# Optimization experiments

Hardware: AMD Instinct MI355X
Metric: run time of the kernel (lower is better)

## Reference

```python
import jax, jax.numpy as jnp
import numpy as np

N_CLASSES = 3  # hardcoded in the original module (labels == 0/1/2)
EPS = 1e-12    # F.normalize default eps


def setup_inputs() -> dict:
    key = jax.random.key(0)
    k1, k2, k3 = jax.random.split(key, 3)
    query = jax.random.normal(k1, (32768, 256), dtype=jnp.float32)
    memory = jax.random.normal(k2, (3, 512, 256), dtype=jnp.float32)
    labels = jax.random.randint(k3, (32768,), 0, 3, dtype=jnp.int64)
    return {"query": query, "labels": labels, "memory": memory}


def reference(query, labels, memory):
    C, n_cells, d = memory.shape  # (3, 512, 256)
    # ---- read: cross-attention over all C*n_cells memory slots ----
    mem_flat = memory.reshape(C * n_cells, d)
    scores = jax.nn.softmax(query @ mem_flat.T, axis=1)  # (N, C*n_cells)
    q_read = scores @ mem_flat                           # (N, d) == the per-row loop, batched

    # ---- update (training path): masked softmax over queries per class ----
    def upd(c):
        mask = labels == c                               # (N,)
        logits = query @ memory[c].T                     # (N, n_cells)
        logits = jnp.where(mask[:, None], logits, -jnp.inf)
        sq = jax.nn.softmax(logits, axis=0)              # softmax over (masked) queries
        delta = sq.T @ query                             # (n_cells, d); zero rows contribute 0
        new = memory[c] + delta
        norm = jnp.maximum(jnp.linalg.norm(new, axis=1, keepdims=True), EPS)
        return new / norm                                # F.normalize over dim=1

    new_mem = jnp.stack([upd(c) for c in range(C)])      # C is a small fixed constant (3)
    return q_read, jax.lax.stop_gradient(new_mem)        # original detaches updated memory
```

## Files before the change

kernel.cpp:

```cpp
#include <hip/hip_runtime.h>
#include <math.h>

#define NQ    32768
#define DDIM  256
#define NCLS  3
#define CELLS 512
#define STOT  1536
#define BK    32

typedef __attribute__((ext_vector_type(8)))  short bf16x8;
typedef __attribute__((ext_vector_type(16))) float f32x16;

#define ROWF(r) (((r) & 3) + 8 * ((r) >> 2) + 4 * lh)

#define PIPE_WAIT_BAR(N) asm volatile("s_waitcnt vmcnt(" #N ")\n\ts_barrier" ::: "memory")
#define PIPE_BAR()       asm volatile("s_barrier" ::: "memory")

__device__ __forceinline__ f32x16 mfma16(bf16x8 a, bf16x8 b, f32x16 c) {
    return __builtin_amdgcn_mfma_f32_32x32x16_bf16(a, b, c, 0, 0, 0);
}
__device__ __forceinline__ unsigned short f2bf(float f) {
    const unsigned u = __float_as_uint(f);
    return (unsigned short)((u + 0x7FFFu + ((u >> 16) & 1u)) >> 16);
}
__device__ __forceinline__ float bf2f(unsigned short b) {
    return __uint_as_float(((unsigned)b) << 16);
}
__device__ __forceinline__ void gl16(const unsigned short* g, unsigned short* l) {
    __builtin_amdgcn_global_load_lds(
        (const __attribute__((address_space(1))) unsigned int*)g,
        (__attribute__((address_space(3))) unsigned int*)l, 16, 0, 0);
}

__global__ __launch_bounds__(256) void k_convert(const float* __restrict__ src,
        unsigned short* __restrict__ hi, unsigned short* __restrict__ lo,
        unsigned short* __restrict__ hiT, float* __restrict__ sq, int R) {
    __shared__ unsigned short lh_s[64][65];
    const int r0 = blockIdx.x * 64, k0 = blockIdx.y * 64, t = threadIdx.x;
#pragma unroll
    for (int it = 0; it < 4; ++it) {
        const int idx = t + 256 * it;
        const int rl = idx >> 4, kq = idx & 15;
        const float4 v = *(const float4*)(src + (size_t)(r0 + rl) * DDIM + k0 + kq * 4);
        const unsigned short h0 = f2bf(v.x), h1 = f2bf(v.y), h2 = f2bf(v.z), h3 = f2bf(v.w);
        const unsigned short l0 = f2bf(v.x - bf2f(h0)), l1 = f2bf(v.y - bf2f(h1));
        const unsigned short l2 = f2bf(v.z - bf2f(h2)), l3 = f2bf(v.w - bf2f(h3));
        ushort4 hv; hv.x = h0; hv.y = h1; hv.z = h2; hv.w = h3;
        ushort4 lv; lv.x = l0; lv.y = l1; lv.z = l2; lv.w = l3;
        *(ushort4*)(hi + (size_t)(r0 + rl) * DDIM + k0 + kq * 4) = hv;
        *(ushort4*)(lo + (size_t)(r0 + rl) * DDIM + k0 + kq * 4) = lv;
        lh_s[rl][kq * 4 + 0] = h0; lh_s[rl][kq * 4 + 1] = h1;
        lh_s[rl][kq * 4 + 2] = h2; lh_s[rl][kq * 4 + 3] = h3;
        float ssq = v.x * v.x + v.y * v.y + v.z * v.z + v.w * v.w;
        ssq += __shfl_xor(ssq, 1, 64);
        ssq += __shfl_xor(ssq, 2, 64);
        ssq += __shfl_xor(ssq, 4, 64);
        ssq += __shfl_xor(ssq, 8, 64);
        if (kq == 0) atomicAdd(&sq[r0 + rl], ssq);
    }
    __syncthreads();
#pragma unroll
    for (int it = 0; it < 16; ++it) {
        const int idx = t + 256 * it;
        const int kl = idx >> 6, rl = idx & 63;
        hiT[(size_t)(k0 + kl) * R + r0 + rl] = lh_s[rl][kl];
    }
}

__global__ __launch_bounds__(256) void k_pe(
        const unsigned short* __restrict__ Qhi, const unsigned short* __restrict__ Qlo,
        const unsigned short* __restrict__ Mhi, const unsigned short* __restrict__ Mlo,
        const int* __restrict__ labels, const float* __restrict__ qn2,
        const float* __restrict__ mn2,
        unsigned short* __restrict__ P, unsigned short* __restrict__ ET,
        int ibase, int ch, int ipg) {
    __shared__ unsigned short smem[2][2][2][128][BK];
    typedef unsigned short trt[32][40];
    trt* trP = (trt*)&smem[0][0][0][0][0];
    trt* trE = trP + 4;

    const int t = threadIdx.x, lane = t & 63, wid = t >> 6;
    const int l31 = lane & 31, lh = lane >> 5;
    const int wi = wid >> 1, wj = wid & 1;
    int ib, jb;
    if (ipg > 0) {
        const int xcd = blockIdx.x & 7, s = blockIdx.x >> 3;
        jb = s % 12; ib = xcd * ipg + s / 12;
    } else { jb = blockIdx.x % 12; ib = blockIdx.x / 12; }
    const int iblk = ib * 128, jblk = jb * 128;
    const int iloc0 = iblk + wi * 64;
    const int j0    = jblk + wj * 64;
    const int cblk  = jb >> 2;

    const int c0 = wid * 128 + lane, c1 = c0 + 64;
    const int r0 = c0 >> 2, o0 = ((c0 ^ (c0 >> 3)) & 3) * 8;
    const int r1 = c1 >> 2, o1 = ((c1 ^ (c1 >> 3)) & 3) * 8;
    const unsigned short* gA[2] = { Qhi + (size_t)(ibase + iblk) * DDIM,
                                    Qlo + (size_t)(ibase + iblk) * DDIM };
    const unsigned short* gB[2] = { Mhi + (size_t)jblk * DDIM,
                                    Mlo + (size_t)jblk * DDIM };
    auto STAGE = [&](int b, int k0) {
#pragma unroll
        for (int h = 0; h < 2; ++h) {
            gl16(gA[h] + (size_t)r0 * DDIM + k0 + o0, &smem[b][0][h][0][0] + c0 * 8);
            gl16(gA[h] + (size_t)r1 * DDIM + k0 + o1, &smem[b][0][h][0][0] + c1 * 8);
            gl16(gB[h] + (size_t)r0 * DDIM + k0 + o0, &smem[b][1][h][0][0] + c0 * 8);
            gl16(gB[h] + (size_t)r1 * DDIM + k0 + o1, &smem[b][1][h][0][0] + c1 * 8);
        }
    };

    f32x16 acc[2][2] = {};
    const int ra0 = wi * 64 + l31, ra1 = ra0 + 32;
    const int rb0 = wj * 64 + l31, rb1 = rb0 + 32;
    const int swa = (ra0 >> 1) & 3;
    const int swb = (rb0 >> 1) & 3;
    auto COMPUTE = [&](int b) {
#pragma unroll
        for (int t16 = 0; t16 < 2; ++t16) {
            const int oc = t16 * 2 + lh;
            const int ka = (oc ^ swa) * 8, kb = (oc ^ swb) * 8;
            const bf16x8 a0h = *(const bf16x8*)&smem[b][0][0][ra0][ka];
            const bf16x8 a1h = *(const bf16x8*)&smem[b][0][0][ra1][ka];
            const bf16x8 a0l = *(const bf16x8*)&smem[b][0][1][ra0][ka];
            const bf16x8 a1l = *(const bf16x8*)&smem[b][0][1][ra1][ka];
            const bf16x8 b0h = *(const bf16x8*)&smem[b][1][0][rb0][kb];
            const bf16x8 b1h = *(const bf16x8*)&smem[b][1][0][rb1][kb];
            const bf16x8 b0l = *(const bf16x8*)&smem[b][1][1][rb0][kb];
            const bf16x8 b1l = *(const bf16x8*)&smem[b][1][1][rb1][kb];
            acc[0][0] = mfma16(a0h, b0h, acc[0][0]);
            acc[0][0] = mfma16(a0h, b0l, acc[0][0]);
            acc[0][0] = mfma16(a0l, b0h, acc[0][0]);
            acc[0][1] = mfma16(a0h, b1h, acc[0][1]);
            acc[0][1] = mfma16(a0h, b1l, acc[0][1]);
            acc[0][1] = mfma16(a0l, b1h, acc[0][1]);
            acc[1][0] = mfma16(a1h, b0h, acc[1][0]);
            acc[1][0] = mfma16(a1h, b0l, acc[1][0]);
            acc[1][0] = mfma16(a1l, b0h, acc[1][0]);
            acc[1][1] = mfma16(a1h, b1h, acc[1][1]);
            acc[1][1] = mfma16(a1h, b1l, acc[1][1]);
            acc[1][1] = mfma16(a1l, b1h, acc[1][1]);
        }
    };

    STAGE(0, 0);
    STAGE(1, BK);
    for (int s = 0; s < DDIM / BK - 1; ++s) {
        PIPE_WAIT_BAR(8);
        COMPUTE(s & 1);
        PIPE_BAR();
        if (s + 2 < DDIM / BK) STAGE(s & 1, (s + 2) * BK);
    }
    PIPE_WAIT_BAR(0);
    COMPUTE(1);
    __syncthreads();

#pragma unroll
    for (int ti = 0; ti < 2; ++ti) {
        float qn[16]; unsigned lm = 0;
        const int ig0 = ibase + iloc0 + ti * 32;
#pragma unroll
        for (int r = 0; r < 16; ++r) {
            const int ir = ig0 + ROWF(r);
            qn[r] = 6.0f * sqrtf(qn2[ir]);
            lm |= (unsigned)(labels[ir] == cblk) << r;
        }
#pragma unroll
        for (int tj = 0; tj < 2; ++tj) {
            const int jg = j0 + tj * 32 + l31;
            const float mn = 6.0f * sqrtf(mn2[jg]);
#pragma unroll
            for (int r = 0; r < 16; ++r) {
                const float lg = acc[ti][tj][r];
                trP[wid][ROWF(r)][l31] = f2bf(__expf(lg - qn[r]));
                const float e = ((lm >> r) & 1u) ? __expf(lg - mn) : 0.0f;
                trE[wid][l31][ROWF(r)] = f2bf(e);
            }
            const int rr = lane >> 1, off = (lane & 1) * 16;
            {
                const unsigned short* lp = &trP[wid][rr][off];
                const bf16x8 w0 = *(const bf16x8*)(lp);
                const bf16x8 w1 = *(const bf16x8*)(lp + 8);
                unsigned short* prow = P + (size_t)(iloc0 + ti * 32 + rr) * STOT
                                         + j0 + tj * 32 + off;
                *(bf16x8*)(prow)     = w0;
                *(bf16x8*)(prow + 8) = w1;
            }
            {
                const unsigned short* lp = &trE[wid][rr][off];
                const bf16x8 w0 = *(const bf16x8*)(lp);
                const bf16x8 w1 = *(const bf16x8*)(lp + 8);
                unsigned short* erow = ET + (size_t)(j0 + tj * 32 + rr) * ch
                                          + iloc0 + ti * 32 + off;
                *(bf16x8*)(erow)     = w0;
                *(bf16x8*)(erow + 8) = w1;
            }
        }
    }
}

__global__ __launch_bounds__(256) void k_pv(const unsigned short* __restrict__ P,
        const unsigned short* __restrict__ MhiT,
        float* __restrict__ out, int ibase) {
    __shared__ unsigned short sP[2][64][64];
    __shared__ unsigned short sV[2][128][64];
    const int t = threadIdx.x, lane = t & 63, wid = t >> 6;
    const int l31 = lane & 31, lh = lane >> 5;
    const int wq = wid >> 1, wd = wid & 1;
    const int qblk = blockIdx.x * 64, dblk = blockIdx.y * 128;
    const int d0 = dblk + wd * 64;
    const unsigned short* gP = P + (size_t)qblk * STOT;
    const unsigned short* gV = MhiT + (size_t)dblk * STOT;

    auto STAGE = [&](int b, int k0) {
#pragma unroll
        for (int it = 0; it < 2; ++it) {
            const int c = wid * 128 + it * 64 + lane;
            const int r = c >> 3, o = ((c & 7) ^ (r & 7)) * 8;
            gl16(gP + (size_t)r * STOT + k0 + o, &sP[b][0][0] + c * 8);
        }
#pragma unroll
        for (int it = 0; it < 4; ++it) {
            const int c = wid * 256 + it * 64 + lane;
            const int r = c >> 3, o = ((c & 7) ^ (r & 7)) * 8;
            gl16(gV + (size_t)r * STOT + k0 + o, &sV[b][0][0] + c * 8);
        }
    };

    bf16x8 bones;
    const short ob = (l31 == 0) ? (short)0x3F80 : (short)0;
#pragma unroll
    for (int e = 0; e < 8; ++e) bones[e] = ob;

    f32x16 acc[2] = {};
    f32x16 accS = {};
    const int rp = wq * 32 + l31, rv0 = wd * 64 + l31, rv1 = rv0 + 32;
    auto COMPUTE = [&](int b) {
#pragma unroll
        for (int t16 = 0; t16 < 4; ++t16) {
            const int oc = t16 * 2 + lh;
            const bf16x8 a0 = *(const bf16x8*)&sP[b][rp][(oc ^ (rp & 7)) * 8];
            const bf16x8 b0 = *(const bf16x8*)&sV[b][rv0][(oc ^ (rv0 & 7)) * 8];
            const bf16x8 b1 = *(const bf16x8*)&sV[b][rv1][(oc ^ (rv1 & 7)) * 8];
            acc[0] = mfma16(a0, b0, acc[0]);
            acc[1] = mfma16(a0, b1, acc[1]);
            accS   = mfma16(a0, bones, accS);
        }
    };

    STAGE(0, 0);
    STAGE(1, 64);
    for (int s = 0; s < STOT / 64 - 1; ++s) {
        PIPE_WAIT_BAR(6);
        COMPUTE(s & 1);
        PIPE_BAR();
        if (s + 2 < STOT / 64) STAGE(s & 1, (s + 2) * 64);
    }
    PIPE_WAIT_BAR(0);
    COMPUTE(1);

    float rinv[16];
#pragma unroll
    for (int r = 0; r < 16; ++r) rinv[r] = 1.f / __shfl(accS[r], lh << 5, 64);
#pragma unroll
    for (int td = 0; td < 2; ++td) {
#pragma unroll
        for (int r = 0; r < 16; ++r) {
            const int ig = ibase + qblk + wq * 32 + ROWF(r);
            out[(size_t)ig * DDIM + d0 + td * 32 + l31] = acc[td][r] * rinv[r];
        }
    }
}

__global__ __launch_bounds__(256) void k_delta4(const unsigned short* __restrict__ ET,
        const unsigned short* __restrict__ QhiT,
        float* __restrict__ delta, float* __restrict__ colsum,
        int ibase, int ch, int ppx) {
    __shared__ unsigned short sE[2][128][64];
    __shared__ unsigned short sQ[2][128][64];
    const int t = threadIdx.x, lane = t & 63, wid = t >> 6;
    const int l31 = lane & 31, lh = lane >> 5;
    const int wj = wid >> 1, wd = wid & 1;
    int jb, db, kb;
    if (ppx > 0) {
        const int xcd = blockIdx.x & 7, s = blockIdx.x >> 3;
        jb = s % 12;
        const int pidx = xcd * ppx + s / 12;
        kb = pidx >> 1; db = pidx & 1;
    } else {
        jb = blockIdx.x % 12; db = (blockIdx.x / 12) & 1; kb = blockIdx.x / 24;
    }
    const int jblk = jb * 128, dblk = db * 128, i0 = kb * 1024;
    const int j0 = jblk + wj * 64, d0 = dblk + wd * 64;
    const unsigned short* gE = ET + (size_t)jblk * ch + i0;
    const unsigned short* gQ = QhiT + (size_t)dblk * NQ + ibase + i0;

    auto STAGE = [&](int b, int k0) {
#pragma unroll
        for (int it = 0; it < 4; ++it) {
            const int c = wid * 256 + it * 64 + lane;
            const int r = c >> 3, o = ((c & 7) ^ (r & 7)) * 8;
            gl16(gE + (size_t)r * ch + k0 + o, &sE[b][0][0] + c * 8);
            gl16(gQ + (size_t)r * NQ + k0 + o, &sQ[b][0][0] + c * 8);
        }
    };

    bf16x8 bones;
    const short ob = (l31 == 0) ? (short)0x3F80 : (short)0;
#pragma unroll
    for (int e = 0; e < 8; ++e) bones[e] = ob;

    f32x16 acc[2][2] = {};
    f32x16 accS0 = {}, accS1 = {};
    const int re0 = wj * 64 + l31, re1 = re0 + 32;
    const int rq0 = wd * 64 + l31, rq1 = rq0 + 32;
    auto COMPUTE = [&](int b) {
#pragma unroll
        for (int t16 = 0; t16 < 4; ++t16) {
            const int oc = t16 * 2 + lh;
            const bf16x8 a0 = *(const bf16x8*)&sE[b][re0][(oc ^ (re0 & 7)) * 8];
            const bf16x8 a1 = *(const bf16x8*)&sE[b][re1][(oc ^ (re1 & 7)) * 8];
            const bf16x8 b0 = *(const bf16x8*)&sQ[b][rq0][(oc ^ (rq0 & 7)) * 8];
            const bf16x8 b1 = *(const bf16x8*)&sQ[b][rq1][(oc ^ (rq1 & 7)) * 8];
            acc[0][0] = mfma16(a0, b0, acc[0][0]);
            acc[0][1] = mfma16(a0, b1, acc[0][1]);
            acc[1][0] = mfma16(a1, b0, acc[1][0]);
            acc[1][1] = mfma16(a1, b1, acc[1][1]);
            if (wd == 0) {
                accS0 = mfma16(a0, bones, accS0);
                accS1 = mfma16(a1, bones, accS1);
            }
        }
    };

    STAGE(0, 0);
    STAGE(1, 64);
    for (int s = 0; s < 15; ++s) {
        PIPE_WAIT_BAR(8);
        COMPUTE(s & 1);
        PIPE_BAR();
        if (s + 2 < 16) STAGE(s & 1, (s + 2) * 64);
    }
    PIPE_WAIT_BAR(0);
    COMPUTE(1);

#pragma unroll
    for (int tj = 0; tj < 2; ++tj) {
#pragma unroll
        for (int td = 0; td < 2; ++td) {
#pragma unroll
            for (int r = 0; r < 16; ++r) {
                const int jr = j0 + tj * 32 + ROWF(r);
                atomicAdd(&delta[(size_t)jr * DDIM + d0 + td * 32 + l31], acc[tj][td][r]);
            }
        }
    }
    if (wd == 0 && l31 == 0) {
#pragma unroll
        for (int r = 0; r < 16; ++r) {
            atomicAdd(&colsum[j0 + ROWF(r)], accS0[r]);
            atomicAdd(&colsum[j0 + 32 + ROWF(r)], accS1[r]);
        }
    }
}

__global__ void k_final(const float* __restrict__ M,
                        const float* __restrict__ delta,
                        const float* __restrict__ colsum,
                        float* __restrict__ out) {
    const int row  = blockIdx.x * 4 + (threadIdx.x >> 6);
    const int lane = threadIdx.x & 63;
    const float inv = 1.f / colsum[row];
    const float4 mv = *(const float4*)(M + (size_t)row * DDIM + lane * 4);
    const float4 dv = *(const float4*)(delta + (size_t)row * DDIM + lane * 4);
    float4 nv;
    nv.x = fmaf(dv.x, inv, mv.x);
    nv.y = fmaf(dv.y, inv, mv.y);
    nv.z = fmaf(dv.z, inv, mv.z);
    nv.w = fmaf(dv.w, inv, mv.w);
    float ss = nv.x * nv.x + nv.y * nv.y + nv.z * nv.z + nv.w * nv.w;
#pragma unroll
    for (int sh = 1; sh < 64; sh <<= 1) ss += __shfl_xor(ss, sh, 64);
    const float rn = 1.f / fmaxf(sqrtf(ss), 1e-12f);
    nv.x *= rn; nv.y *= rn; nv.z *= rn; nv.w *= rn;
    *(float4*)(out + (size_t)NQ * DDIM + (size_t)row * DDIM + lane * 4) = nv;
}

extern "C" void kernel_launch(void* const* d_in, const int* in_sizes, int n_in,
                              void* d_out, int out_size, void* d_ws, size_t ws_size,
                              hipStream_t stream) {
    const float* Q      = (const float*)d_in[0];
    const int*   labels = (const int*)d_in[1];
    const float* M      = (const float*)d_in[2];
    float* out = (float*)d_out;

    char* p = (char*)d_ws;
    float* colsum = (float*)p;          p += (size_t)STOT * 4;
    float* delta  = (float*)p;          p += (size_t)STOT * DDIM * 4;
    float* qn2    = (float*)p;          p += (size_t)NQ * 4;
    float* mn2    = (float*)p;          p += (size_t)STOT * 4;
    const size_t zero_bytes = (size_t)(p - (char*)d_ws);
    unsigned short* Qhi  = (unsigned short*)p; p += (size_t)NQ * DDIM * 2;
    unsigned short* Qlo  = (unsigned short*)p; p += (size_t)NQ * DDIM * 2;
    unsigned short* QhiT = (unsigned short*)p; p += (size_t)NQ * DDIM * 2;
    unsigned short* Mhi  = (unsigned short*)p; p += (size_t)STOT * DDIM * 2;
    unsigned short* Mlo  = (unsigned short*)p; p += (size_t)STOT * DDIM * 2;
    unsigned short* MhiT = (unsigned short*)p; p += (size_t)STOT * DDIM * 2;
    const size_t fixed_bytes = (size_t)(p - (char*)d_ws);

    int nch = 2;
    while (nch < 32 &&
           fixed_bytes + (size_t)(NQ / nch) * STOT * 2 * 2 > ws_size) nch <<= 1;
    const int ch = NQ / nch;
    unsigned short* Pbuf = (unsigned short*)p;
    unsigned short* ETb  = Pbuf + (size_t)ch * STOT;

    const int ipg    = ((ch / 128) % 8 == 0) ? (ch / 128) / 8 : 0;
    const int ksplit = ch / 1024;
    const int ppx    = ((2 * ksplit) % 8 == 0) ? (2 * ksplit) / 8 : 0;

    hipMemsetAsync(d_ws, 0, zero_bytes, stream);

    k_convert<<<dim3(NQ / 64, 4), 256, 0, stream>>>(Q, Qhi, Qlo, QhiT, qn2, NQ);
    k_convert<<<dim3(STOT / 64, 4), 256, 0, stream>>>(M, Mhi, Mlo, MhiT, mn2, STOT);

    for (int h = 0; h < nch; ++h) {
        const int ibase = h * ch;
        k_pe<<<12 * (ch / 128), 256, 0, stream>>>(Qhi, Qlo, Mhi, Mlo, labels,
                                                  qn2, mn2, Pbuf, ETb, ibase, ch, ipg);
        k_pv<<<dim3(ch / 64, 2), 256, 0, stream>>>(Pbuf, MhiT, out, ibase);
        k_delta4<<<24 * ksplit, 256, 0, stream>>>(ETb, QhiT, delta, colsum,
                                                  ibase, ch, ppx);
    }
    k_final<<<STOT / 4, 256, 0, stream>>>(M, delta, colsum, out);
}
```

Before: 295.9 us.

## Compute softmax row/column sums in k_pe epilogue and enlarge k_pv tile

Row sums of P and column sums of E are now accumulated with atomics in the k_pe epilogue, taken from the bf16 values just written. This removes the extra ones-vector MFMAs from k_pv and k_delta4. k_pv's query tile grows from 64 to 128 rows with a 2x2 MFMA accumulator per wave, which improves reuse of the staged V tiles and halves its grid. The cost is many more global atomics in k_pe, an extra rowsum buffer that has to be zeroed, and higher register and LDS use in k_pv.

```diff
diff --git a/kernel.cpp b/kernel.cpp
--- a/kernel.cpp
+++ b/kernel.cpp
@@ -25,6 +25,13 @@
 }
 __device__ __forceinline__ float bf2f(unsigned short b) {
     return __uint_as_float(((unsigned)b) << 16);
+}
+__device__ __forceinline__ float sum16(bf16x8 w0, bf16x8 w1) {
+    float s = 0.f;
+#pragma unroll
+    for (int e = 0; e < 8; ++e)
+        s += bf2f((unsigned short)w0[e]) + bf2f((unsigned short)w1[e]);
+    return s;
 }
 __device__ __forceinline__ void gl16(const unsigned short* g, unsigned short* l) {
     __builtin_amdgcn_global_load_lds(
@@ -73,6 +80,7 @@
         const int* __restrict__ labels, const float* __restrict__ qn2,
         const float* __restrict__ mn2,
         unsigned short* __restrict__ P, unsigned short* __restrict__ ET,
+        float* __restrict__ rowsum, float* __restrict__ colsum,
         int ibase, int ch, int ipg) {
     __shared__ unsigned short smem[2][2][2][128][BK];
     typedef unsigned short trt[32][40];
@@ -184,6 +192,7 @@
                                          + j0 + tj * 32 + off;
                 *(bf16x8*)(prow)     = w0;
                 *(bf16x8*)(prow + 8) = w1;
+                atomicAdd(&rowsum[ibase + iloc0 + ti * 32 + rr], sum16(w0, w1));
             }
             {
                 const unsigned short* lp = &trE[wid][rr][off];
@@ -193,64 +202,56 @@
                                           + iloc0 + ti * 32 + off;
                 *(bf16x8*)(erow)     = w0;
                 *(bf16x8*)(erow + 8) = w1;
+                atomicAdd(&colsum[j0 + tj * 32 + rr], sum16(w0, w1));
             }
         }
     }
 }
 
 __global__ __launch_bounds__(256) void k_pv(const unsigned short* __restrict__ P,
-        const unsigned short* __restrict__ MhiT,
+        const unsigned short* __restrict__ MhiT, const float* __restrict__ rowsum,
         float* __restrict__ out, int ibase) {
-    __shared__ unsigned short sP[2][64][64];
+    __shared__ unsigned short sP[2][128][64];
     __shared__ unsigned short sV[2][128][64];
     const int t = threadIdx.x, lane = t & 63, wid = t >> 6;
     const int l31 = lane & 31, lh = lane >> 5;
     const int wq = wid >> 1, wd = wid & 1;
-    const int qblk = blockIdx.x * 64, dblk = blockIdx.y * 128;
-    const int d0 = dblk + wd * 64;
+    const int qblk = blockIdx.x * 128, dblk = blockIdx.y * 128;
     const unsigned short* gP = P + (size_t)qblk * STOT;
     const unsigned short* gV = MhiT + (size_t)dblk * STOT;
 
     auto STAGE = [&](int b, int k0) {
-#pragma unroll
-        for (int it = 0; it < 2; ++it) {
-            const int c = wid * 128 + it * 64 + lane;
-            const int r = c >> 3, o = ((c & 7) ^ (r & 7)) * 8;
-            gl16(gP + (size_t)r * STOT + k0 + o, &sP[b][0][0] + c * 8);
-        }
 #pragma unroll
         for (int it = 0; it < 4; ++it) {
             const int c = wid * 256 + it * 64 + lane;
             const int r = c >> 3, o = ((c & 7) ^ (r & 7)) * 8;
+            gl16(gP + (size_t)r * STOT + k0 + o, &sP[b][0][0] + c * 8);
             gl16(gV + (size_t)r * STOT + k0 + o, &sV[b][0][0] + c * 8);
         }
     };
 
-    bf16x8 bones;
-    const short ob = (l31 == 0) ? (short)0x3F80 : (short)0;
-#pragma unroll
-    for (int e = 0; e < 8; ++e) bones[e] = ob;
-
-    f32x16 acc[2] = {};
-    f32x16 accS = {};
-    const int rp = wq * 32 + l31, rv0 = wd * 64 + l31, rv1 = rv0 + 32;
+    f32x16 acc[2][2] = {};
+    const int rp0 = wq * 64 + l31, rp1 = rp0 + 32;
+    const int rv0 = wd * 64 + l31, rv1 = rv0 + 32;
     auto COMPUTE = [&](int b) {
 #pragma unroll
         for (int t16 = 0; t16 < 4; ++t16) {
             const int oc = t16 * 2 + lh;
-            const bf16x8 a0 = *(const bf16x8*)&sP[b][rp][(oc ^ (rp & 7)) * 8];
+            const bf16x8 a0 = *(const bf16x8*)&sP[b][rp0][(oc ^ (rp0 & 7)) * 8];
+            const bf16x8 a1 = *(const bf16x8*)&sP[b][rp1][(oc ^ (rp1 & 7)) * 8];
             const bf16x8 b0 = *(const bf16x8*)&sV[b][rv0][(oc ^ (rv0 & 7)) * 8];
             const bf16x8 b1 = *(const bf16x8*)&sV[b][rv1][(oc ^ (rv1 & 7)) * 8];
-            acc[0] = mfma16(a0, b0, acc[0]);
-            acc[1] = mfma16(a0, b1, acc[1]);
-            accS   = mfma16(a0, bones, accS);
+            acc[0][0] = mfma16(a0, b0, acc[0][0]);
+            acc[0][1] = mfma16(a0, b1, acc[0][1]);
+            acc[1][0] = mfma16(a1, b0, acc[1][0]);
+            acc[1][1] = mfma16(a1, b1, acc[1][1]);
         }
     };
 
     STAGE(0, 0);
     STAGE(1, 64);
     for (int s = 0; s < STOT / 64 - 1; ++s) {
-        PIPE_WAIT_BAR(6);
+        PIPE_WAIT_BAR(8);
         COMPUTE(s & 1);
         PIPE_BAR();
         if (s + 2 < STOT / 64) STAGE(s & 1, (s + 2) * 64);
@@ -258,23 +259,29 @@
     PIPE_WAIT_BAR(0);
     COMPUTE(1);
 
-    float rinv[16];
-#pragma unroll
-    for (int r = 0; r < 16; ++r) rinv[r] = 1.f / __shfl(accS[r], lh << 5, 64);
-#pragma unroll
-    for (int td = 0; td < 2; ++td) {
-#pragma unroll
-        for (int r = 0; r < 16; ++r) {
-            const int ig = ibase + qblk + wq * 32 + ROWF(r);
-            out[(size_t)ig * DDIM + d0 + td * 32 + l31] = acc[td][r] * rinv[r];
+    float riv[2][16];
+#pragma unroll
+    for (int tq = 0; tq < 2; ++tq)
+#pragma unroll
+        for (int r = 0; r < 16; ++r)
+            riv[tq][r] = 1.f / rowsum[ibase + qblk + wq * 64 + tq * 32 + ROWF(r)];
+#pragma unroll
+    for (int tq = 0; tq < 2; ++tq) {
+#pragma unroll
+        for (int td = 0; td < 2; ++td) {
+#pragma unroll
+            for (int r = 0; r < 16; ++r) {
+                const int ig = ibase + qblk + wq * 64 + tq * 32 + ROWF(r);
+                const int od = dblk + wd * 64 + td * 32 + l31;
+                out[(size_t)ig * DDIM + od] = acc[tq][td][r] * riv[tq][r];
+            }
         }
     }
 }
 
 __global__ __launch_bounds__(256) void k_delta4(const unsigned short* __restrict__ ET,
         const unsigned short* __restrict__ QhiT,
-        float* __restrict__ delta, float* __restrict__ colsum,
-        int ibase, int ch, int ppx) {
+        float* __restrict__ delta, int ibase, int ch, int ppx) {
     __shared__ unsigned short sE[2][128][64];
     __shared__ unsigned short sQ[2][128][64];
     const int t = threadIdx.x, lane = t & 63, wid = t >> 6;
@@ -304,13 +311,7 @@
         }
     };
 
-    bf16x8 bones;
-    const short ob = (l31 == 0) ? (short)0x3F80 : (short)0;
-#pragma unroll
-    for (int e = 0; e < 8; ++e) bones[e] = ob;
-
     f32x16 acc[2][2] = {};
-    f32x16 accS0 = {}, accS1 = {};
     const int re0 = wj * 64 + l31, re1 = re0 + 32;
     const int rq0 = wd * 64 + l31, rq1 = rq0 + 32;
     auto COMPUTE = [&](int b) {
@@ -325,10 +326,6 @@
             acc[0][1] = mfma16(a0, b1, acc[0][1]);
             acc[1][0] = mfma16(a1, b0, acc[1][0]);
             acc[1][1] = mfma16(a1, b1, acc[1][1]);
-            if (wd == 0) {
-                accS0 = mfma16(a0, bones, accS0);
-                accS1 = mfma16(a1, bones, accS1);
-            }
         }
     };
 
@@ -352,13 +349,6 @@
                 const int jr = j0 + tj * 32 + ROWF(r);
                 atomicAdd(&delta[(size_t)jr * DDIM + d0 + td * 32 + l31], acc[tj][td][r]);
             }
-        }
-    }
-    if (wd == 0 && l31 == 0) {
-#pragma unroll
-        for (int r = 0; r < 16; ++r) {
-            atomicAdd(&colsum[j0 + ROWF(r)], accS0[r]);
-            atomicAdd(&colsum[j0 + 32 + ROWF(r)], accS1[r]);
         }
     }
 }
@@ -398,6 +388,7 @@
     float* delta  = (float*)p;          p += (size_t)STOT * DDIM * 4;
     float* qn2    = (float*)p;          p += (size_t)NQ * 4;
     float* mn2    = (float*)p;          p += (size_t)STOT * 4;
+    float* rowsum = (float*)p;          p += (size_t)NQ * 4;
     const size_t zero_bytes = (size_t)(p - (char*)d_ws);
     unsigned short* Qhi  = (unsigned short*)p; p += (size_t)NQ * DDIM * 2;
     unsigned short* Qlo  = (unsigned short*)p; p += (size_t)NQ * DDIM * 2;
@@ -426,10 +417,10 @@
     for (int h = 0; h < nch; ++h) {
         const int ibase = h * ch;
         k_pe<<<12 * (ch / 128), 256, 0, stream>>>(Qhi, Qlo, Mhi, Mlo, labels,
-                                                  qn2, mn2, Pbuf, ETb, ibase, ch, ipg);
-        k_pv<<<dim3(ch / 64, 2), 256, 0, stream>>>(Pbuf, MhiT, out, ibase);
-        k_delta4<<<24 * ksplit, 256, 0, stream>>>(ETb, QhiT, delta, colsum,
-                                                  ibase, ch, ppx);
+                                                  qn2, mn2, Pbuf, ETb, rowsum, colsum,
+                                                  ibase, ch, ipg);
+        k_pv<<<dim3(ch / 128, 2), 256, 0, stream>>>(Pbuf, MhiT, rowsum, out, ibase);
+        k_delta4<<<24 * ksplit, 256, 0, stream>>>(ETb, QhiT, delta, ibase, ch, ppx);
     }
     k_final<<<STOT / 4, 256, 0, stream>>>(M, delta, colsum, out);
 }
```

Result: slower. 633.1 us (+114.0%).
